# Performance work log

Hardware: AMD Instinct MI355X
Metric: run time of the kernel (lower is better)

## Reference

```python
import jax, jax.numpy as jnp
import numpy as np

K = 5          # kernel_size per pseudo-dim
KK = K * K     # 25 weight slots (dim=2)
NUM_GRAPHS = 64


def spline_conv(x, src, dst, pseudo, W, root, bias):
    """SplineConv, degree-1 open B-spline, dim=2, aggr='mean', root weight + bias.
    x: [N, I], pseudo: [E, 2] in [0,1], W: [KK, I, O], root: [I, O], bias: [O].
    """
    N = x.shape[0]
    E = src.shape[0]
    O = W.shape[-1]
    # degree-1 open spline: v = u * (K-1); linear interpolation between knots
    v = pseudo * (K - 1)                      # [E, 2]
    bot = jnp.floor(v)
    frac = v - bot                            # [E, 2]
    bot = bot.astype(jnp.int32)
    # precompute per-node transform for every kernel slot: [N, KK, O] -> flat [N*KK, O]
    Xk = jnp.einsum('ni,kio->nko', x, W).reshape(N * KK, O)
    msg = jnp.zeros((E, O), x.dtype)
    for s0 in (0, 1):
        b0 = frac[:, 0] if s0 else 1.0 - frac[:, 0]
        i0 = jnp.clip(bot[:, 0] + s0, 0, K - 1)
        for s1 in (0, 1):
            b1 = frac[:, 1] if s1 else 1.0 - frac[:, 1]
            i1 = jnp.clip(bot[:, 1] + s1, 0, K - 1)
            flat = src * KK + i0 * K + i1     # [E] gather index into Xk
            msg = msg + (b0 * b1)[:, None] * Xk[flat]
    # mean aggregation over incoming edges
    agg = jax.ops.segment_sum(msg, dst, num_segments=N)
    deg = jax.ops.segment_sum(jnp.ones((E,), x.dtype), dst, num_segments=N)
    agg = agg / jnp.maximum(deg, 1.0)[:, None]
    return agg + x @ root + bias


def batch_average(x, batch, num_graphs):
    s = jax.ops.segment_sum(x, batch, num_segments=num_graphs)
    c = jax.ops.segment_sum(jnp.ones((x.shape[0],), x.dtype), batch, num_segments=num_graphs)
    return s / jnp.maximum(c, 1.0)[:, None]


def setup_inputs() -> dict:
    key = jax.random.key(0)
    ks = jax.random.split(key, 16)
    N, E = 30000, 600000
    x = jax.random.normal(ks[0], (N, 8), dtype=jnp.float32)
    edge_index = jax.random.randint(ks[1], (2, E), 0, N, dtype=jnp.int64)
    pseudo = jax.random.uniform(ks[2], (E, 2), dtype=jnp.float32)
    batch = jnp.sort(jax.random.randint(ks[3], (N,), 0, NUM_GRAPHS, dtype=jnp.int64))

    def glorot(k, shape):
        fan = shape[-2] + shape[-1]
        return jax.random.normal(k, shape, dtype=jnp.float32) * np.sqrt(2.0 / fan)

    return {
        'x': x, 'edge_index': edge_index, 'pseudo': pseudo, 'batch': batch,
        'W1': glorot(ks[4], (KK, 8, 32)),   'root1': glorot(ks[5], (8, 32)),   'b1': jnp.zeros((32,), jnp.float32),
        'W2': glorot(ks[6], (KK, 32, 64)),  'root2': glorot(ks[7], (32, 64)),  'b2': jnp.zeros((64,), jnp.float32),
        'W3': glorot(ks[8], (KK, 64, 124)), 'root3': glorot(ks[9], (64, 124)), 'b3': jnp.zeros((124,), jnp.float32),
        'fc_w': glorot(ks[10], (124, 30)),  'fc_b': jnp.zeros((30,), jnp.float32),
    }


def reference(x, edge_index, pseudo, batch,
              W1, root1, b1, W2, root2, b2, W3, root3, b3, fc_w, fc_b):
    src = edge_index[0].astype(jnp.int32)
    dst = edge_index[1].astype(jnp.int32)
    batch32 = batch.astype(jnp.int32)
    h = jax.nn.elu(spline_conv(x, src, dst, pseudo, W1, root1, b1))
    h = jax.nn.elu(spline_conv(h, src, dst, pseudo, W2, root2, b2))
    h = jax.nn.elu(spline_conv(h, src, dst, pseudo, W3, root3, b3))
    g = batch_average(h, batch32, NUM_GRAPHS)        # [G, 124]
    # dropout is identity in eval mode
    logits = g @ fc_w + fc_b                         # [G, 30]
    return jax.nn.log_softmax(logits, axis=-1)
```

## Files before the change

kernel.cpp:

```cpp
#include <hip/hip_runtime.h>
#include <cstdint>
#include <cstddef>

#define KKSLOTS 25

typedef __attribute__((ext_vector_type(8))) short short8;
typedef __attribute__((ext_vector_type(4))) float f32x4;
typedef __attribute__((ext_vector_type(4))) unsigned short us4;

__device__ __forceinline__ unsigned short f2bf(float f) {
    unsigned u = __float_as_uint(f);
    u += 0x7FFF + ((u >> 16) & 1);
    return (unsigned short)(u >> 16);
}
__device__ __forceinline__ float bf2f(unsigned short b) {
    return __uint_as_float((unsigned)b << 16);
}

__global__ void csr_count_kernel(const int* __restrict__ dst, int* __restrict__ cnt, int E) {
    int e = blockIdx.x * blockDim.x + threadIdx.x;
    if (e < E) atomicAdd(&cnt[dst[e]], 1);
}

#define SCAN_B 256
__global__ __launch_bounds__(SCAN_B) void scan1_kernel(const int* __restrict__ cnt,
                                                       int* __restrict__ off,
                                                       int* __restrict__ bsum, int N) {
    __shared__ int tmp[SCAN_B];
    int g = blockIdx.x * SCAN_B + threadIdx.x;
    int v = (g < N) ? cnt[g] : 0;
    tmp[threadIdx.x] = v;
    __syncthreads();
    for (int d = 1; d < SCAN_B; d <<= 1) {
        int t = (threadIdx.x >= d) ? tmp[threadIdx.x - d] : 0;
        __syncthreads();
        tmp[threadIdx.x] += t;
        __syncthreads();
    }
    if (g < N) off[g] = tmp[threadIdx.x] - v;
    if (threadIdx.x == SCAN_B - 1) bsum[blockIdx.x] = tmp[threadIdx.x];
}

__global__ __launch_bounds__(SCAN_B) void scan2_kernel(int* __restrict__ bsum, int nb) {
    __shared__ int tmp[SCAN_B];
    int v = (threadIdx.x < nb) ? bsum[threadIdx.x] : 0;
    tmp[threadIdx.x] = v;
    __syncthreads();
    for (int d = 1; d < SCAN_B; d <<= 1) {
        int t = (threadIdx.x >= d) ? tmp[threadIdx.x - d] : 0;
        __syncthreads();
        tmp[threadIdx.x] += t;
        __syncthreads();
    }
    if (threadIdx.x < nb) bsum[threadIdx.x] = tmp[threadIdx.x] - v;
}

__global__ void scan3_kernel(int* __restrict__ off, const int* __restrict__ bsum, int N) {
    int g = blockIdx.x * SCAN_B + threadIdx.x;
    if (g < N) off[g] += bsum[blockIdx.x];
}

__global__ void csr_fill_kernel(const int* __restrict__ src, const int* __restrict__ dst,
                                const float* __restrict__ pseudo,
                                int* __restrict__ off, int4* __restrict__ rec, int E) {
    int e = blockIdx.x * blockDim.x + threadIdx.x;
    if (e >= E) return;
    int d = dst[e];
    int p = atomicAdd(&off[d], 1);
    float v0 = pseudo[2 * e + 0] * 4.0f;
    float v1 = pseudo[2 * e + 1] * 4.0f;
    float fl0 = floorf(v0), fl1 = floorf(v1);
    float f0 = v0 - fl0, f1 = v1 - fl1;
    int b0 = (int)fl0, b1 = (int)fl1;
    int i0a = min(max(b0, 0), 4),     i1a = min(max(b1, 0), 4);
    int i0b = min(max(b0 + 1, 0), 4), i1b = min(max(b1 + 1, 0), 4);
    int s00 = i0a * 5 + i1a;
    int s01 = i0a * 5 + i1b;
    int s10 = i0b * 5 + i1a;
    int s11 = i0b * 5 + i1b;
    int packed = s00 | (s01 << 5) | (s10 << 10) | (s11 << 15);
    int4 r;
    r.x = src[e];
    r.y = packed;
    r.z = __float_as_int(f0);
    r.w = __float_as_int(f1);
    rec[p] = r;
}

__global__ void to_bf16_kernel(const float* __restrict__ in, unsigned short* __restrict__ out, int n) {
    int i = blockIdx.x * 256 + threadIdx.x;
    if (i < n) out[i] = f2bf(in[i]);
}

template<int KP, int I, int O, int OP>
__global__ void build_wt_kernel(const float* __restrict__ W, const float* __restrict__ root,
                                unsigned short* __restrict__ WT) {
    int idx = blockIdx.x * 256 + threadIdx.x;
    if (idx >= OP * KP) return;
    int o = idx / KP, k = idx - o * KP;
    float v = 0.0f;
    if (o < O) {
        if (k < KKSLOTS * I) v = W[(size_t)k * O + o];
        else if (k < (KKSLOTS + 1) * I) v = root[(size_t)(k - KKSLOTS * I) * O + o];
    }
    WT[idx] = f2bf(v);
}

template<int I>
__device__ __forceinline__ void edge_proc(float* lat, int chb, int sh, bool selA, bool selB,
                                          int4 r, const unsigned short* __restrict__ xb,
                                          float scale) {
    float f0 = __int_as_float(r.z), f1 = __int_as_float(r.w);
    float w = (selA ? f0 : 1.0f - f0) * (selB ? f1 : 1.0f - f1) * scale;
    int slot = (r.y >> sh) & 31;
    if constexpr (I == 8) {
        float xv = bf2f(xb[(size_t)r.x * 8 + chb]);
        lat[slot * 8 + chb] += w * xv;
    } else {
        us4 xr = *(const us4*)&xb[(size_t)r.x * I + chb];
        float* d = lat + slot * I + chb;
        f32x4 v = *(f32x4*)d;
        v[0] += w * bf2f(xr[0]);
        v[1] += w * bf2f(xr[1]);
        v[2] += w * bf2f(xr[2]);
        v[3] += w * bf2f(xr[3]);
        *(f32x4*)d = v;
    }
}

template<int I, int KP>
__global__ __launch_bounds__(256) void seg_accum_kernel(
        const unsigned short* __restrict__ xb, const int4* __restrict__ rec,
        const int* __restrict__ off, unsigned short* __restrict__ accB,
        int nlo, int nhi) {
    constexpr int SLOTS = KKSLOTS * I;
    constexpr bool DUAL = (I != 64);
    constexpr int TILE = DUAL ? 2 * SLOTS : SLOTS;
    __shared__ __align__(16) float la_all[4][TILE];
    int wline = threadIdx.x >> 6, lane = threadIdx.x & 63;
    float* la = la_all[wline];
    int wid = blockIdx.x * 4 + wline;
    int nwt = gridDim.x << 2;

    int e_lo = (nlo == 0) ? 0 : off[nlo - 1];
    int e_hi = off[nhi - 1];
    long long span = (long long)e_hi - e_lo;
    int t0 = e_lo + (int)(span * wid / nwt);
    int t1 = e_lo + (int)(span * (wid + 1) / nwt);

    int ns, ne;
    {   int lo = nlo, hi = nhi;
        while (lo < hi) { int m = (lo + hi) >> 1; if (off[m] > t0) hi = m; else lo = m + 1; }
        ns = (wid == 0) ? nlo : lo; }
    {   int lo = nlo, hi = nhi;
        while (lo < hi) { int m = (lo + hi) >> 1; if (off[m] > t1) hi = m; else lo = m + 1; }
        ne = (wid == nwt - 1) ? nhi : lo; }
    if (ns >= ne) return;

    int corner, chb;
    float* lat;
    if constexpr (I == 64)      { corner = lane >> 4;        chb = (lane & 15) * 4; lat = la; }
    else if constexpr (I == 32) { corner = (lane >> 3) & 3;  chb = (lane & 7) * 4;  lat = la + (lane >> 5) * SLOTS; }
    else                        { corner = (lane >> 3) & 3;  chb = lane & 7;        lat = la + (lane >> 5) * SLOTS; }
    int sh = corner * 5;
    bool selA = (corner & 2) != 0, selB = (corner & 1) != 0;
    int h = lane >> 5;

    for (int t = lane; t < TILE; t += 64) la[t] = 0.0f;

    int j = (ns == 0) ? 0 : off[ns - 1];
    for (int n = ns; n < ne; ++n) {
        int je = off[n];
        int jstart = j;
        if constexpr (!DUAL) {
            while (j + 2 <= je) {
                int4 r0 = rec[j], r1 = rec[j + 1];
                edge_proc<I>(lat, chb, sh, selA, selB, r0, xb, 1.0f);
                edge_proc<I>(lat, chb, sh, selA, selB, r1, xb, 1.0f);
                j += 2;
            }
            if (j < je) { edge_proc<I>(lat, chb, sh, selA, selB, rec[j], xb, 1.0f); ++j; }
        } else {
            while (j < je) {
                int idx = j + h;
                int cl = min(idx, je - 1);
                int4 r = rec[cl];
                float scale = (idx < je) ? 1.0f : 0.0f;
                edge_proc<I>(lat, chb, sh, selA, selB, r, xb, scale);
                j += 2;
            }
            j = je;
        }

        float dinv = 1.0f / fmaxf((float)(je - jstart), 1.0f);
        unsigned* drow = (unsigned*)(accB + (size_t)(n - nlo) * KP);
        const unsigned* hrow = (const unsigned*)(xb + (size_t)n * I);
        for (int t = lane; t < KP / 2; t += 64) {
            int e0 = 2 * t;
            if (e0 < SLOTS) {
                float v0 = la[e0], v1 = la[e0 + 1];
                if constexpr (DUAL) { v0 += la[SLOTS + e0]; v1 += la[SLOTS + e0 + 1]; }
                v0 *= dinv; v1 *= dinv;
                drow[t] = (unsigned)f2bf(v0) | ((unsigned)f2bf(v1) << 16);
            } else {
                int ii = e0 - SLOTS;
                drow[t] = (ii < I) ? hrow[ii >> 1] : 0u;
            }
        }
        for (int t = lane; t < TILE; t += 64) la[t] = 0.0f;
    }
}

template<int KP, int O, int OP>
__global__ __launch_bounds__(256) void contract_mfma_kernel(
        const unsigned short* __restrict__ accB, const unsigned short* __restrict__ WT,
        const float* __restrict__ bias, unsigned short* __restrict__ hout,
        int nlo, int nhi) {
    constexpr int NF = OP / 16;
    constexpr int LDW = 40;
    __shared__ unsigned short wTl[OP][LDW];
    int tid = threadIdx.x;
    int wv = tid >> 6, lane = tid & 63;
    int quad = lane >> 4, l16 = lane & 15;
    int n0 = nlo + blockIdx.x * 64;

    int an = n0 + wv * 16 + l16;
    int arow = min(an, nhi - 1) - nlo;

    f32x4 acc[NF];
    #pragma unroll
    for (int t = 0; t < NF; ++t) acc[t] = (f32x4){0.0f, 0.0f, 0.0f, 0.0f};

    for (int k0 = 0; k0 < KP; k0 += 32) {
        for (int t = tid; t < OP * 8; t += 256) {
            int o = t >> 3;
            int kk = (t & 7) * 4;
            *(us4*)&wTl[o][kk] = *(const us4*)&WT[(size_t)o * KP + k0 + kk];
        }
        __syncthreads();
        short8 a = *(const short8*)(accB + (size_t)arow * KP + k0 + quad * 8);
        #pragma unroll
        for (int t = 0; t < NF; ++t) {
            short8 b = *(const short8*)&wTl[t * 16 + l16][quad * 8];
            acc[t] = __builtin_amdgcn_mfma_f32_16x16x32_bf16(a, b, acc[t], 0, 0, 0);
        }
        __syncthreads();
    }

    #pragma unroll
    for (int t = 0; t < NF; ++t) {
        int o = t * 16 + l16;
        if (o >= O) continue;
        float bs = bias[o];
        #pragma unroll
        for (int r = 0; r < 4; ++r) {
            int n = n0 + wv * 16 + quad * 4 + r;
            if (n >= nhi) continue;
            float v = acc[t][r] + bs;
            v = (v > 0.0f) ? v : expm1f(v);
            hout[(size_t)n * O + o] = f2bf(v);
        }
    }
}

#define GS_CH 128
__global__ __launch_bounds__(128) void graph_reduce_kernel(
        const unsigned short* __restrict__ h3, const int* __restrict__ batch,
        float* __restrict__ g, float* __restrict__ cnt, int N) {
    int o = threadIdx.x;
    int n0 = blockIdx.x * GS_CH;
    int n1 = min(n0 + GS_CH, N);
    if (o < 124) {
        float local = 0.0f;
        int cur_b = batch[n0];
        for (int n = n0; n < n1; ++n) {
            int b = batch[n];
            if (b != cur_b) {
                atomicAdd(&g[cur_b * 124 + o], local);
                local = 0.0f;
                cur_b = b;
            }
            local += bf2f(h3[(size_t)n * 124 + o]);
        }
        atomicAdd(&g[cur_b * 124 + o], local);
    } else if (o == 124) {
        float localc = 0.0f;
        int cur_b = batch[n0];
        for (int n = n0; n < n1; ++n) {
            int b = batch[n];
            if (b != cur_b) {
                atomicAdd(&cnt[cur_b], localc);
                localc = 0.0f;
                cur_b = b;
            }
            localc += 1.0f;
        }
        atomicAdd(&cnt[cur_b], localc);
    }
}

__global__ void head_kernel(const float* __restrict__ g, const float* __restrict__ cnt,
                            const float* __restrict__ fcw, const float* __restrict__ fcb,
                            float* __restrict__ out) {
    __shared__ float logits[32];
    __shared__ float red[2];
    int b = blockIdx.x;
    int o = threadIdx.x;
    float c = fmaxf(cnt[b], 1.0f);
    if (o < 30) {
        float a = fcb[o];
        for (int i = 0; i < 124; ++i)
            a = fmaf(g[b * 124 + i] / c, fcw[i * 30 + o], a);
        logits[o] = a;
    }
    __syncthreads();
    if (o == 0) {
        float m = -1e30f;
        for (int j = 0; j < 30; ++j) m = fmaxf(m, logits[j]);
        float s = 0.0f;
        for (int j = 0; j < 30; ++j) s += expf(logits[j] - m);
        red[0] = m;
        red[1] = logf(s);
    }
    __syncthreads();
    if (o < 30) out[b * 30 + o] = logits[o] - red[0] - red[1];
}

template<int I, int O, int OP>
static void run_layer(const unsigned short* hb, const unsigned short* WT, const float* bias,
                      unsigned short* hout, unsigned short* accB,
                      const int4* rec, const int* off,
                      int N, size_t avail, hipStream_t stream) {
    constexpr int KP = ((26 * I + 31) / 32) * 32;
    size_t perNode = (size_t)KP * 2;
    size_t maxNodesS = avail / perNode;
    int maxNodes = (maxNodesS > (size_t)N) ? N : (int)maxNodesS;
    if (maxNodes < 64) maxNodes = 64;
    for (int nlo = 0; nlo < N; nlo += maxNodes) {
        int nhi = nlo + maxNodes;
        if (nhi > N) nhi = N;
        int cn = nhi - nlo;
        seg_accum_kernel<I, KP><<<2048, 256, 0, stream>>>(hb, rec, off, accB, nlo, nhi);
        contract_mfma_kernel<KP, O, OP><<<(cn + 63) / 64, 256, 0, stream>>>(
            accB, WT, bias, hout, nlo, nhi);
    }
}

extern "C" void kernel_launch(void* const* d_in, const int* in_sizes, int n_in,
                              void* d_out, int out_size, void* d_ws, size_t ws_size,
                              hipStream_t stream) {
    const float* x      = (const float*)d_in[0];
    const int*   ei     = (const int*)  d_in[1];
    const float* pseudo = (const float*)d_in[2];
    const int*   batch  = (const int*)  d_in[3];
    const float* W1 = (const float*)d_in[4];
    const float* r1 = (const float*)d_in[5];
    const float* b1 = (const float*)d_in[6];
    const float* W2 = (const float*)d_in[7];
    const float* r2 = (const float*)d_in[8];
    const float* b2 = (const float*)d_in[9];
    const float* W3 = (const float*)d_in[10];
    const float* r3 = (const float*)d_in[11];
    const float* b3 = (const float*)d_in[12];
    const float* fcw = (const float*)d_in[13];
    const float* fcb = (const float*)d_in[14];

    int N = in_sizes[0] / 8;
    int E = in_sizes[1] / 2;
    const int* srcp = ei;
    const int* dstp = ei + E;

    constexpr int KP1 = 224, KP2 = 832, KP3 = 1664;

    char* p = (char*)d_ws;
    unsigned short* xb  = (unsigned short*)p; p += (size_t)N * 8 * 2;
    unsigned short* h1  = (unsigned short*)p; p += (size_t)N * 32 * 2;
    unsigned short* h2  = (unsigned short*)p; p += (size_t)N * 64 * 2;
    unsigned short* h3  = (unsigned short*)p; p += (size_t)N * 124 * 2;
    float* gbuf = (float*)p; p += 64 * 124 * 4;
    float* cntF = (float*)p; p += 256;
    int*   cntI = (int*)p;   p += ((size_t)N * 4 + 15) & ~15ULL;
    int*   off  = (int*)p;   p += ((size_t)N * 4 + 15) & ~15ULL;
    int*   bsum = (int*)p;   p += SCAN_B * 4;
    int4*  rec  = (int4*)p;  p += (size_t)E * 16;
    unsigned short* WT1 = (unsigned short*)p; p += (size_t)32  * KP1 * 2;
    unsigned short* WT2 = (unsigned short*)p; p += (size_t)64  * KP2 * 2;
    unsigned short* WT3 = (unsigned short*)p; p += (size_t)128 * KP3 * 2;
    unsigned short* accB = (unsigned short*)p;
    size_t used = (size_t)(p - (char*)d_ws);
    size_t avail = (ws_size > used) ? (ws_size - used) : 0;

    hipMemsetAsync(gbuf, 0, 64 * 124 * 4 + 256 + (((size_t)N * 4 + 15) & ~15ULL), stream);

    int nb_scan = (N + SCAN_B - 1) / SCAN_B;
    csr_count_kernel<<<(E + 255) / 256, 256, 0, stream>>>(dstp, cntI, E);
    scan1_kernel<<<nb_scan, SCAN_B, 0, stream>>>(cntI, off, bsum, N);
    scan2_kernel<<<1, SCAN_B, 0, stream>>>(bsum, nb_scan);
    scan3_kernel<<<nb_scan, SCAN_B, 0, stream>>>(off, bsum, N);
    csr_fill_kernel<<<(E + 255) / 256, 256, 0, stream>>>(srcp, dstp, pseudo, off, rec, E);

    to_bf16_kernel<<<(N * 8 + 255) / 256, 256, 0, stream>>>(x, xb, N * 8);
    build_wt_kernel<KP1, 8,  32,  32 ><<<(32  * KP1 + 255) / 256, 256, 0, stream>>>(W1, r1, WT1);
    build_wt_kernel<KP2, 32, 64,  64 ><<<(64  * KP2 + 255) / 256, 256, 0, stream>>>(W2, r2, WT2);
    build_wt_kernel<KP3, 64, 124, 128><<<(128 * KP3 + 255) / 256, 256, 0, stream>>>(W3, r3, WT3);

    run_layer<8,  32,  32 >(xb, WT1, b1, h1, accB, rec, off, N, avail, stream);
    run_layer<32, 64,  64 >(h1, WT2, b2, h2, accB, rec, off, N, avail, stream);
    run_layer<64, 124, 128>(h2, WT3, b3, h3, accB, rec, off, N, avail, stream);

    graph_reduce_kernel<<<(N + GS_CH - 1) / GS_CH, 128, 0, stream>>>(h3, batch, gbuf, cntF, N);
    head_kernel<<<64, 64, 0, stream>>>(gbuf, cntF, fcw, fcb, (float*)d_out);
}
```

Measured before the change: 558.1 us.

## Precompute fp16 corner weights and scatter edges via LDS atomics; drop LDS weight staging

The CSR fill kernel now stores the four bilinear corner weights as packed fp16 values instead of the raw fractions. The segment-accumulate kernel drops its per-corner lane mapping and dual tiles: each lane owns one channel, processes 64/I edges per wave step and adds all four corners with shared-memory atomics. This removes the duplicate-tile reduction and the per-lane weight math, but adds LDS atomic contention and fp16 weight rounding. The MFMA contraction kernel reads weights straight from global memory instead of staging them in LDS, which removes two block barriers per K step and relies on cache for reuse.

```diff
diff --git a/kernel.cpp b/kernel.cpp
--- a/kernel.cpp
+++ b/kernel.cpp
@@ -1,4 +1,5 @@
 #include <hip/hip_runtime.h>
+#include <hip/hip_fp16.h>
 #include <cstdint>
 #include <cstddef>
 
@@ -15,6 +16,14 @@
 }
 __device__ __forceinline__ float bf2f(unsigned short b) {
     return __uint_as_float((unsigned)b << 16);
+}
+__device__ __forceinline__ unsigned pack_h2(float a, float b) {
+    unsigned short ha = __half_as_ushort(__float2half_rn(a));
+    unsigned short hb = __half_as_ushort(__float2half_rn(b));
+    return (unsigned)ha | ((unsigned)hb << 16);
+}
+__device__ __forceinline__ float h2f(unsigned short u) {
+    return __half2float(__ushort_as_half(u));
 }
 
 __global__ void csr_count_kernel(const int* __restrict__ dst, int* __restrict__ cnt, int E) {
@@ -78,12 +87,12 @@
     int s01 = i0a * 5 + i1b;
     int s10 = i0b * 5 + i1a;
     int s11 = i0b * 5 + i1b;
-    int packed = s00 | (s01 << 5) | (s10 << 10) | (s11 << 15);
+    float g0 = 1.0f - f0, g1 = 1.0f - f1;
     int4 r;
     r.x = src[e];
-    r.y = packed;
-    r.z = __float_as_int(f0);
-    r.w = __float_as_int(f1);
+    r.y = s00 | (s01 << 5) | (s10 << 10) | (s11 << 15);
+    r.z = (int)pack_h2(g0 * g1, g0 * f1);
+    r.w = (int)pack_h2(f0 * g1, f0 * f1);
     rec[p] = r;
 }
 
@@ -106,37 +115,14 @@
     WT[idx] = f2bf(v);
 }
 
-template<int I>
-__device__ __forceinline__ void edge_proc(float* lat, int chb, int sh, bool selA, bool selB,
-                                          int4 r, const unsigned short* __restrict__ xb,
-                                          float scale) {
-    float f0 = __int_as_float(r.z), f1 = __int_as_float(r.w);
-    float w = (selA ? f0 : 1.0f - f0) * (selB ? f1 : 1.0f - f1) * scale;
-    int slot = (r.y >> sh) & 31;
-    if constexpr (I == 8) {
-        float xv = bf2f(xb[(size_t)r.x * 8 + chb]);
-        lat[slot * 8 + chb] += w * xv;
-    } else {
-        us4 xr = *(const us4*)&xb[(size_t)r.x * I + chb];
-        float* d = lat + slot * I + chb;
-        f32x4 v = *(f32x4*)d;
-        v[0] += w * bf2f(xr[0]);
-        v[1] += w * bf2f(xr[1]);
-        v[2] += w * bf2f(xr[2]);
-        v[3] += w * bf2f(xr[3]);
-        *(f32x4*)d = v;
-    }
-}
-
 template<int I, int KP>
 __global__ __launch_bounds__(256) void seg_accum_kernel(
         const unsigned short* __restrict__ xb, const int4* __restrict__ rec,
         const int* __restrict__ off, unsigned short* __restrict__ accB,
         int nlo, int nhi) {
     constexpr int SLOTS = KKSLOTS * I;
-    constexpr bool DUAL = (I != 64);
-    constexpr int TILE = DUAL ? 2 * SLOTS : SLOTS;
-    __shared__ __align__(16) float la_all[4][TILE];
+    constexpr int EPW = 64 / I;
+    __shared__ float la_all[4][SLOTS];
     int wline = threadIdx.x >> 6, lane = threadIdx.x & 63;
     float* la = la_all[wline];
     int wid = blockIdx.x * 4 + wline;
@@ -157,57 +143,46 @@
         ne = (wid == nwt - 1) ? nhi : lo; }
     if (ns >= ne) return;
 
-    int corner, chb;
-    float* lat;
-    if constexpr (I == 64)      { corner = lane >> 4;        chb = (lane & 15) * 4; lat = la; }
-    else if constexpr (I == 32) { corner = (lane >> 3) & 3;  chb = (lane & 7) * 4;  lat = la + (lane >> 5) * SLOTS; }
-    else                        { corner = (lane >> 3) & 3;  chb = lane & 7;        lat = la + (lane >> 5) * SLOTS; }
-    int sh = corner * 5;
-    bool selA = (corner & 2) != 0, selB = (corner & 1) != 0;
-    int h = lane >> 5;
-
-    for (int t = lane; t < TILE; t += 64) la[t] = 0.0f;
+    int h  = lane / I;
+    int ch = lane % I;
+
+    for (int t = lane; t < SLOTS; t += 64) la[t] = 0.0f;
 
     int j = (ns == 0) ? 0 : off[ns - 1];
     for (int n = ns; n < ne; ++n) {
         int je = off[n];
         int jstart = j;
-        if constexpr (!DUAL) {
-            while (j + 2 <= je) {
-                int4 r0 = rec[j], r1 = rec[j + 1];
-                edge_proc<I>(lat, chb, sh, selA, selB, r0, xb, 1.0f);
-                edge_proc<I>(lat, chb, sh, selA, selB, r1, xb, 1.0f);
-                j += 2;
-            }
-            if (j < je) { edge_proc<I>(lat, chb, sh, selA, selB, rec[j], xb, 1.0f); ++j; }
-        } else {
-            while (j < je) {
-                int idx = j + h;
-                int cl = min(idx, je - 1);
-                int4 r = rec[cl];
-                float scale = (idx < je) ? 1.0f : 0.0f;
-                edge_proc<I>(lat, chb, sh, selA, selB, r, xb, scale);
-                j += 2;
-            }
-            j = je;
-        }
+        for (; j < je; j += EPW) {
+            int idx = j + h;
+            int cl = min(idx, je - 1);
+            int4 r = rec[cl];
+            float scale = (idx < je) ? 1.0f : 0.0f;
+            float xv = bf2f(xb[(size_t)r.x * I + ch]) * scale;
+            unsigned wz = (unsigned)r.z, ww = (unsigned)r.w;
+            unsigned pk = (unsigned)r.y;
+            unsafeAtomicAdd(&la[((pk      ) & 31) * I + ch], h2f((unsigned short)(wz & 0xFFFF)) * xv);
+            unsafeAtomicAdd(&la[((pk >> 5 ) & 31) * I + ch], h2f((unsigned short)(wz >> 16))    * xv);
+            unsafeAtomicAdd(&la[((pk >> 10) & 31) * I + ch], h2f((unsigned short)(ww & 0xFFFF)) * xv);
+            unsafeAtomicAdd(&la[((pk >> 15) & 31) * I + ch], h2f((unsigned short)(ww >> 16))    * xv);
+        }
+        j = je;
 
         float dinv = 1.0f / fmaxf((float)(je - jstart), 1.0f);
         unsigned* drow = (unsigned*)(accB + (size_t)(n - nlo) * KP);
         const unsigned* hrow = (const unsigned*)(xb + (size_t)n * I);
         for (int t = lane; t < KP / 2; t += 64) {
             int e0 = 2 * t;
+            unsigned outv;
             if (e0 < SLOTS) {
-                float v0 = la[e0], v1 = la[e0 + 1];
-                if constexpr (DUAL) { v0 += la[SLOTS + e0]; v1 += la[SLOTS + e0 + 1]; }
-                v0 *= dinv; v1 *= dinv;
-                drow[t] = (unsigned)f2bf(v0) | ((unsigned)f2bf(v1) << 16);
+                float v0 = la[e0] * dinv, v1 = la[e0 + 1] * dinv;
+                outv = (unsigned)f2bf(v0) | ((unsigned)f2bf(v1) << 16);
             } else {
                 int ii = e0 - SLOTS;
-                drow[t] = (ii < I) ? hrow[ii >> 1] : 0u;
+                outv = (ii < I) ? hrow[ii >> 1] : 0u;
             }
-        }
-        for (int t = lane; t < TILE; t += 64) la[t] = 0.0f;
+            drow[t] = outv;
+        }
+        for (int t = lane; t < SLOTS; t += 64) la[t] = 0.0f;
     }
 }
 
@@ -217,8 +192,6 @@
         const float* __restrict__ bias, unsigned short* __restrict__ hout,
         int nlo, int nhi) {
     constexpr int NF = OP / 16;
-    constexpr int LDW = 40;
-    __shared__ unsigned short wTl[OP][LDW];
     int tid = threadIdx.x;
     int wv = tid >> 6, lane = tid & 63;
     int quad = lane >> 4, l16 = lane & 15;
@@ -226,25 +199,24 @@
 
     int an = n0 + wv * 16 + l16;
     int arow = min(an, nhi - 1) - nlo;
+    const unsigned short* Ap = accB + (size_t)arow * KP + quad * 8;
+
+    const unsigned short* Bp[NF];
+    #pragma unroll
+    for (int t = 0; t < NF; ++t)
+        Bp[t] = WT + (size_t)(t * 16 + l16) * KP + quad * 8;
 
     f32x4 acc[NF];
     #pragma unroll
     for (int t = 0; t < NF; ++t) acc[t] = (f32x4){0.0f, 0.0f, 0.0f, 0.0f};
 
     for (int k0 = 0; k0 < KP; k0 += 32) {
-        for (int t = tid; t < OP * 8; t += 256) {
-            int o = t >> 3;
-            int kk = (t & 7) * 4;
-            *(us4*)&wTl[o][kk] = *(const us4*)&WT[(size_t)o * KP + k0 + kk];
-        }
-        __syncthreads();
-        short8 a = *(const short8*)(accB + (size_t)arow * KP + k0 + quad * 8);
+        short8 a = *(const short8*)(Ap + k0);
         #pragma unroll
         for (int t = 0; t < NF; ++t) {
-            short8 b = *(const short8*)&wTl[t * 16 + l16][quad * 8];
+            short8 b = *(const short8*)(Bp[t] + k0);
             acc[t] = __builtin_amdgcn_mfma_f32_16x16x32_bf16(a, b, acc[t], 0, 0, 0);
         }
-        __syncthreads();
     }
 
     #pragma unroll
```

Result: slower. 1.698 ms (+204.3%).
